# Optimization experiments

Measured on AMD Instinct MI355X. Metric: run time of the kernel, lower is better.

The kernel has to match this reference:

```python
import jax, jax.numpy as jnp
import numpy as np

jax.config.update("jax_enable_x64", True)

NUM_OF_LSB_TO_IGNORE = 5
COMPARISON_NUM_BITS_IGNORED = 5
SCALE = 65536.0  # activations live on an integer-share-like scale so bit shifts matter

BLOCK_SIZES = np.array([[0, 1]] * 32 + [[2, 2]] * 48 + [[4, 4]] * 48)
# active (non-identity) block sizes and the channel indices they own
ACTIVE = [(tuple(int(v) for v in bs), np.where(np.all(BLOCK_SIZES == bs, axis=1))[0])
          for bs in np.unique(BLOCK_SIZES, axis=0) if 0 not in bs]


def setup_inputs() -> dict:
    key = jax.random.key(0)
    activation = jax.random.normal(key, (16, 128, 114, 114), dtype=jnp.float32) * SCALE
    return {"activation": activation}


def _block_sign(x, bh, bw):
    # x: [N, c, H, W]. Pad bottom/right to block multiples, space-to-depth,
    # integer floor-mean per block, LSB truncation via int16 wrap, sign >= 0.
    N, c, H, W = x.shape
    ph, pw = (-H) % bh, (-W) % bw
    xp = jnp.pad(x, ((0, 0), (0, 0), (0, ph), (0, pw)))
    xr = xp.reshape(N, c, (H + ph) // bh, bh, (W + pw) // bw, bw)
    s = xr.sum(axis=(3, 5)).astype(jnp.int64)          # block sums
    mean = s // (bh * bw)                               # integer floor mean
    q = ((mean >> NUM_OF_LSB_TO_IGNORE).astype(jnp.int16)
         .astype(jnp.int64)) << COMPARISON_NUM_BITS_IGNORED
    sign = q >= 0                                       # DReLU
    # broadcast block sign back to pixels, then unpad
    sign = jnp.repeat(jnp.repeat(sign, bh, axis=2), bw, axis=3)
    return sign[:, :, :H, :W]


def reference(activation):
    out = activation
    for (bh, bw), ch in ACTIVE:  # small fixed set of block-size groups
        cur = activation[:, ch]
        sign = _block_sign(cur, bh, bw)
        out = out.at[:, ch].set(cur * sign.astype(activation.dtype))
    return out
```

## Files before the change

kernel.cpp:

```cpp
#include <hip/hip_runtime.h>


typedef float v4 __attribute__((ext_vector_type(4)));

#define PLANE 12996
#define P4 3249

__global__ __launch_bounds__(256) void sbrelu_plane_kernel(const float* __restrict__ in,
                                                           float* __restrict__ out) {
    __shared__ float Lp[PLANE];
    __shared__ float Lm[P4];
    const int wg  = blockIdx.x;
    const int c   = wg & 127;
    const int tid = threadIdx.x;
    const v4* __restrict__ ip = (const v4*)(in + (size_t)wg * PLANE);
    v4* __restrict__       op = (v4*)(out + (size_t)wg * PLANE);

    if (c < 32) {
        v4 r[12];
#pragma unroll
        for (int i = 0; i < 12; ++i) r[i] = ip[tid + 256 * i];
        v4 rt;
        if (tid < 177) rt = ip[tid + 3072];
#pragma unroll
        for (int i = 0; i < 12; ++i) __builtin_nontemporal_store(r[i], &op[tid + 256 * i]);
        if (tid < 177) __builtin_nontemporal_store(rt, &op[tid + 3072]);
        return;
    }

    {
        v4 r[12];
#pragma unroll
        for (int i = 0; i < 12; ++i) r[i] = ip[tid + 256 * i];
        v4 rt;
        if (tid < 177) rt = ip[tid + 3072];
#pragma unroll
        for (int i = 0; i < 12; ++i) *(v4*)&Lp[4 * (tid + 256 * i)] = r[i];
        if (tid < 177) *(v4*)&Lp[4 * (tid + 3072)] = rt;
    }
    __syncthreads();

    if (c < 80) {
        for (int b = tid; b < 3249; b += 256) {
            int bh = b / 57, bw = b - bh * 57;
            const float* p = &Lp[228 * bh + 2 * bw];
            float s = ((p[0] + p[1]) + p[114]) + p[115];
            Lm[b] = (s > -1.0f) ? 1.0f : 0.0f;
        }
    } else {
        for (int b = tid; b < 841; b += 256) {
            int bh = b / 29, bw = b - bh * 29;
            int h0 = 4 * bh, w0 = 4 * bw;
            int nh = (bh == 28) ? 2 : 4;
            int nw = (bw == 28) ? 2 : 4;
            float s = 0.0f;
            for (int r2 = 0; r2 < nh; ++r2) {
                const float* p = &Lp[(h0 + r2) * 114 + w0];
                for (int j = 0; j < nw; ++j) s += p[j];
            }
            Lm[b] = (s > -1.0f) ? 1.0f : 0.0f;
        }
    }
    __syncthreads();

    if (c < 80) {
        for (int i = tid; i < 3249; i += 256) {
            v4 v = *(const v4*)&Lp[4 * i];
            int q = 4 * i;
            int h = q / 114;
            int w = q - h * 114;
            v4 o;
#pragma unroll
            for (int e = 0; e < 4; ++e) {
                o[e] = v[e] * Lm[(h >> 1) * 57 + (w >> 1)];
                ++w;
                if (w == 114) { w = 0; ++h; }
            }
            __builtin_nontemporal_store(o, &op[i]);
        }
    } else {
        for (int i = tid; i < 3249; i += 256) {
            v4 v = *(const v4*)&Lp[4 * i];
            int q = 4 * i;
            int h = q / 114;
            int w = q - h * 114;
            v4 o;
#pragma unroll
            for (int e = 0; e < 4; ++e) {
                o[e] = v[e] * Lm[(h >> 2) * 29 + (w >> 2)];
                ++w;
                if (w == 114) { w = 0; ++h; }
            }
            __builtin_nontemporal_store(o, &op[i]);
        }
    }
}

extern "C" void kernel_launch(void* const* d_in, const int* in_sizes, int n_in,
                              void* d_out, int out_size, void* d_ws, size_t ws_size,
                              hipStream_t stream) {
    const float* in = (const float*)d_in[0];
    float* out = (float*)d_out;
    sbrelu_plane_kernel<<<2048, 256, 0, stream>>>(in, out);
}
```

Before: 190.4 us.

## Split into mask-compute kernel and elementwise apply kernel via byte workspace

Replaces the single per-plane kernel with two launches. The first reads only the 96 blocked channels per sample and writes per-block sign masks as bytes into workspace. The second is a flat elementwise kernel that re-reads the input, looks up the mask and writes the output. The aim is higher parallelism and occupancy by dropping the large per-block LDS footprint from the apply pass, at the cost of re-reading 75% of the input, an extra launch, and a workspace round trip.

```diff
diff --git a/kernel.cpp b/kernel.cpp
--- a/kernel.cpp
+++ b/kernel.cpp
@@ -5,49 +5,37 @@
 
 #define PLANE 12996
 #define P4 3249
+#define WS4_BASE 2495232
 
-__global__ __launch_bounds__(256) void sbrelu_plane_kernel(const float* __restrict__ in,
-                                                           float* __restrict__ out) {
+__global__ __launch_bounds__(256) void mask_kernel(const float* __restrict__ in,
+                                                   unsigned char* __restrict__ ws) {
     __shared__ float Lp[PLANE];
-    __shared__ float Lm[P4];
     const int wg  = blockIdx.x;
-    const int c   = wg & 127;
+    const int n   = wg / 96;
+    const int cr  = wg - n * 96;
     const int tid = threadIdx.x;
-    const v4* __restrict__ ip = (const v4*)(in + (size_t)wg * PLANE);
-    v4* __restrict__       op = (v4*)(out + (size_t)wg * PLANE);
+    const v4* __restrict__ ip = (const v4*)(in + (size_t)(n * 128 + 32 + cr) * PLANE);
 
-    if (c < 32) {
-        v4 r[12];
+    v4 r[12];
 #pragma unroll
-        for (int i = 0; i < 12; ++i) r[i] = ip[tid + 256 * i];
-        v4 rt;
-        if (tid < 177) rt = ip[tid + 3072];
+    for (int i = 0; i < 12; ++i) r[i] = ip[tid + 256 * i];
+    v4 rt;
+    if (tid < 177) rt = ip[tid + 3072];
 #pragma unroll
-        for (int i = 0; i < 12; ++i) __builtin_nontemporal_store(r[i], &op[tid + 256 * i]);
-        if (tid < 177) __builtin_nontemporal_store(rt, &op[tid + 3072]);
-        return;
-    }
-
-    {
-        v4 r[12];
-#pragma unroll
-        for (int i = 0; i < 12; ++i) r[i] = ip[tid + 256 * i];
-        v4 rt;
-        if (tid < 177) rt = ip[tid + 3072];
-#pragma unroll
-        for (int i = 0; i < 12; ++i) *(v4*)&Lp[4 * (tid + 256 * i)] = r[i];
-        if (tid < 177) *(v4*)&Lp[4 * (tid + 3072)] = rt;
-    }
+    for (int i = 0; i < 12; ++i) *(v4*)&Lp[4 * (tid + 256 * i)] = r[i];
+    if (tid < 177) *(v4*)&Lp[4 * (tid + 3072)] = rt;
     __syncthreads();
 
-    if (c < 80) {
+    if (cr < 48) {
+        unsigned char* mp = ws + (size_t)(n * 48 + cr) * 3249;
         for (int b = tid; b < 3249; b += 256) {
             int bh = b / 57, bw = b - bh * 57;
             const float* p = &Lp[228 * bh + 2 * bw];
             float s = ((p[0] + p[1]) + p[114]) + p[115];
-            Lm[b] = (s > -1.0f) ? 1.0f : 0.0f;
+            mp[b] = (s > -1.0f) ? 1 : 0;
         }
     } else {
+        unsigned char* mp = ws + WS4_BASE + (size_t)(n * 48 + (cr - 48)) * 841;
         for (int b = tid; b < 841; b += 256) {
             int bh = b / 29, bw = b - bh * 29;
             int h0 = 4 * bh, w0 = 4 * bw;
@@ -58,42 +46,43 @@
                 const float* p = &Lp[(h0 + r2) * 114 + w0];
                 for (int j = 0; j < nw; ++j) s += p[j];
             }
-            Lm[b] = (s > -1.0f) ? 1.0f : 0.0f;
+            mp[b] = (s > -1.0f) ? 1 : 0;
         }
     }
-    __syncthreads();
+}
 
-    if (c < 80) {
-        for (int i = tid; i < 3249; i += 256) {
-            v4 v = *(const v4*)&Lp[4 * i];
-            int q = 4 * i;
-            int h = q / 114;
-            int w = q - h * 114;
-            v4 o;
+__global__ __launch_bounds__(256) void apply_kernel(const float* __restrict__ in,
+                                                    const unsigned char* __restrict__ ws,
+                                                    float* __restrict__ out) {
+    const int i = blockIdx.x * 256 + threadIdx.x;
+    v4 v = ((const v4*)in)[i];
+    int plane = i / P4;
+    int rr    = i - plane * P4;
+    int c     = plane & 127;
+    v4 o;
+    if (c < 32) {
+        o = v;
+    } else {
+        int q = 4 * rr;
+        int h = q / 114;
+        int w = q - h * 114;
+        if (c < 80) {
+            const unsigned char* mp = ws + (size_t)((plane >> 7) * 48 + (c - 32)) * 3249;
 #pragma unroll
             for (int e = 0; e < 4; ++e) {
-                o[e] = v[e] * Lm[(h >> 1) * 57 + (w >> 1)];
-                ++w;
-                if (w == 114) { w = 0; ++h; }
+                o[e] = v[e] * (float)mp[(h >> 1) * 57 + (w >> 1)];
+                if (++w == 114) { w = 0; ++h; }
             }
-            __builtin_nontemporal_store(o, &op[i]);
-        }
-    } else {
-        for (int i = tid; i < 3249; i += 256) {
-            v4 v = *(const v4*)&Lp[4 * i];
-            int q = 4 * i;
-            int h = q / 114;
-            int w = q - h * 114;
-            v4 o;
+        } else {
+            const unsigned char* mp = ws + WS4_BASE + (size_t)((plane >> 7) * 48 + (c - 80)) * 841;
 #pragma unroll
             for (int e = 0; e < 4; ++e) {
-                o[e] = v[e] * Lm[(h >> 2) * 29 + (w >> 2)];
-                ++w;
-                if (w == 114) { w = 0; ++h; }
+                o[e] = v[e] * (float)mp[(h >> 2) * 29 + (w >> 2)];
+                if (++w == 114) { w = 0; ++h; }
             }
-            __builtin_nontemporal_store(o, &op[i]);
         }
     }
+    __builtin_nontemporal_store(o, &((v4*)out)[i]);
 }
 
 extern "C" void kernel_launch(void* const* d_in, const int* in_sizes, int n_in,
@@ -101,5 +90,7 @@
                               hipStream_t stream) {
     const float* in = (const float*)d_in[0];
     float* out = (float*)d_out;
-    sbrelu_plane_kernel<<<2048, 256, 0, stream>>>(in, out);
+    unsigned char* ws = (unsigned char*)d_ws;
+    mask_kernel<<<1536, 256, 0, stream>>>(in, ws);
+    apply_kernel<<<25992, 256, 0, stream>>>(in, ws, out);
 }
```

Result: slower. 195.3 us (+2.6%).
